# Performance work log

Measured on AMD Instinct MI355X. Metric: run time of the kernel, lower is better.

The kernel has to match this reference:

```python
import jax, jax.numpy as jnp
import numpy as np

TEAM = 5
N_PLAYER = 131072
PD = 256
HD = 256
MLP_H = 512
B = 16384

def _combine(t=TEAM):
    i1, i2 = [], []
    for i in range(t):
        for j in range(t):
            if i != j:
                i1.append(i); i2.append(j)
    return np.array(i1), np.array(i2)

IDX1, IDX2 = _combine()

def setup_inputs() -> dict:
    key = jax.random.key(0)
    ks = jax.random.split(key, 12)
    def xavier(k, shape):
        fan_in, fan_out = shape[1], shape[0]
        std = np.sqrt(2.0 / (fan_in + fan_out))
        return (jax.random.normal(k, shape, dtype=jnp.float32) * std)
    return {
        'team_ids': jax.random.randint(ks[0], (B, TEAM), 0, N_PLAYER),
        'emb': xavier(ks[1], (N_PLAYER, PD)),
        'fm_w1': xavier(ks[2], (2 * HD, PD)),
        'fm_b1': jnp.zeros((2 * HD,), jnp.float32),
        'fm_w2': xavier(ks[3], (HD, 2 * HD)),
        'fm_b2': jnp.zeros((HD,), jnp.float32),
        'att_w': xavier(ks[4], (HD, HD)),
        'att_b': jnp.zeros((HD,), jnp.float32),
        'mlp_w1': xavier(ks[5], (MLP_H, HD)),
        'mlp_b1': jnp.zeros((MLP_H,), jnp.float32),
        'mlp_w2': xavier(ks[6], (1, MLP_H)),
        'mlp_b2': jnp.zeros((1,), jnp.float32),
    }

def reference(team_ids, emb, fm_w1, fm_b1, fm_w2, fm_b2, att_w, att_b,
              mlp_w1, mlp_b1, mlp_w2, mlp_b2):
    # embedding lookup: [B, 5, PD]
    x = emb[team_ids]
    # feature mapper: Linear -> SiLU -> Linear  => [B, 5, HD]
    h = jax.nn.silu(jnp.einsum('btp,hp->bth', x, fm_w1) + fm_b1)
    h = jnp.einsum('bth,oh->bto', h, fm_w2) + fm_b2
    # pairwise gather (20 ordered pairs): [B, 20, HD]
    a = h[:, IDX1]
    b = h[:, IDX2]
    prod = a * b
    # small MLP (dropout is inference identity): [B, 20]
    m = jax.nn.silu(jnp.einsum('bph,mh->bpm', prod, mlp_w1) + mlp_b1)
    order2 = (jnp.einsum('bpm,om->bpo', m, mlp_w2) + mlp_b2)[..., 0]
    # attention (reduce=True -> view [B, 5, 4, HD], softmax over axis 2)
    wa = jnp.einsum('bph,oh->bpo', a, att_w) + att_b
    score = (wa * b).sum(-1).reshape(-1, TEAM, TEAM - 1)
    normal = jax.nn.softmax(score, axis=2).reshape(-1, TEAM * (TEAM - 1))
    order2 = order2 * normal
    return order2.sum(axis=1, keepdims=True)  # [B, 1]
```

## Files before the change

### kernel.cpp

```cpp
#include <hip/hip_runtime.h>

#define NB     16384
#define TEAM   5
#define NPAIR  20
#define UPAIR  10
#define PD     256
#define HD     256
#define H1D    512
#define NPLAY  (NB*TEAM)
#define NCHUNK 4

typedef __attribute__((ext_vector_type(4))) float f32x4;
typedef __attribute__((ext_vector_type(8))) short s16x8;

__device__ __forceinline__ float silu_f(float x){ return x / (1.0f + __expf(-x)); }

__device__ __forceinline__ unsigned short bf16_rne(float x){
  unsigned u = __float_as_uint(x);
  unsigned r = u + 0x7fffu + ((u >> 16) & 1u);
  return (unsigned short)(r >> 16);
}
__device__ __forceinline__ float bf16_to_f(unsigned short s){
  return __uint_as_float(((unsigned)s) << 16);
}

__global__ void k_pack(const float* __restrict__ w, short* __restrict__ wf,
                       int KT, int total)
{
  const int tid = blockIdx.x * 256 + threadIdx.x;
  if (tid >= total) return;
  const int slot = tid & 7;
  const int lane = (tid >> 3) & 63;
  const int grp  = tid >> 9;
  const int kt   = grp % KT;
  const int nt   = grp / KT;
  const int K    = KT * 32;
  const int n = nt * 16 + (lane & 15);
  const int k = kt * 32 + ((lane >> 4) << 3) + slot;
  const float v = w[(size_t)n * K + k];
  const unsigned short hi = bf16_rne(v);
  const float lo = v - bf16_to_f(hi);
  wf[tid]         = (short)hi;
  wf[total + tid] = (short)bf16_rne(lo);
}

__global__ __launch_bounds__(256) void k_fm4(
    const int* __restrict__ tids, const float* __restrict__ emb,
    const short* __restrict__ w1f, const float* __restrict__ b1,
    const short* __restrict__ w2f, const float* __restrict__ b2,
    float* __restrict__ Hout)
{
  __shared__ char smem[65536 + 3072];
  short* Af  = reinterpret_cast<short*>(smem);
  short* H1f = reinterpret_cast<short*>(smem);
  float* Bb  = reinterpret_cast<float*>(smem + 65536);

  const int t = threadIdx.x, lane = t & 63, w = t >> 6;
  const int m0 = blockIdx.x * 32;

  Bb[t]       = b1[t];
  Bb[t + 256] = b1[t + 256];
  Bb[t + 512] = b2[t];

  #pragma unroll
  for (int f = 0; f < 8; ++f) {
    const int g     = t + f * 256;
    const int sg    = (g & 1) * 4;
    const int lane_ = (g >> 1) & 63;
    const int kt_   = (g >> 7) & 7;
    const int mt_   = g >> 10;
    const int p     = mt_ * 16 + (lane_ & 15);
    const int k     = kt_ * 32 + ((lane_ >> 4) << 3) + sg;
    const int row   = tids[m0 + p];
    const float4 a4 = *reinterpret_cast<const float4*>(emb + (size_t)row * PD + k);
    float pv[4] = {a4.x, a4.y, a4.z, a4.w};
    short hi[4], lo[4];
    #pragma unroll
    for (int e = 0; e < 4; ++e) {
      const unsigned short h = bf16_rne(pv[e]);
      hi[e] = (short)h;
      lo[e] = (short)bf16_rne(pv[e] - bf16_to_f(h));
    }
    const int off = ((mt_*8 + kt_)*64 + lane_)*8 + sg;
    *reinterpret_cast<short4*>(&Af[off])        = make_short4(hi[0],hi[1],hi[2],hi[3]);
    *reinterpret_cast<short4*>(&Af[8192 + off]) = make_short4(lo[0],lo[1],lo[2],lo[3]);
  }
  __syncthreads();

  const s16x8* B1 = reinterpret_cast<const s16x8*>(w1f);
  const s16x8* B2 = reinterpret_cast<const s16x8*>(w2f);

  f32x4 acc1[2][8];
  #pragma unroll
  for (int mt = 0; mt < 2; ++mt)
    #pragma unroll
    for (int j = 0; j < 8; ++j) acc1[mt][j] = (f32x4){0.f,0.f,0.f,0.f};

  #pragma unroll
  for (int kt = 0; kt < 8; ++kt) {
    s16x8 ah[2], al[2];
    #pragma unroll
    for (int mt = 0; mt < 2; ++mt) {
      ah[mt] = *reinterpret_cast<const s16x8*>(&Af[((mt*8 + kt)*64 + lane)*8]);
      al[mt] = *reinterpret_cast<const s16x8*>(&Af[8192 + ((mt*8 + kt)*64 + lane)*8]);
    }
    #pragma unroll
    for (int j = 0; j < 8; ++j) {
      const int nt = w * 8 + j;
      const s16x8 bh = B1[(nt*8 + kt)*64 + lane];
      const s16x8 bl = B1[16384 + (nt*8 + kt)*64 + lane];
      #pragma unroll
      for (int mt = 0; mt < 2; ++mt) {
        acc1[mt][j] = __builtin_amdgcn_mfma_f32_16x16x32_bf16(ah[mt], bh, acc1[mt][j], 0,0,0);
        acc1[mt][j] = __builtin_amdgcn_mfma_f32_16x16x32_bf16(al[mt], bh, acc1[mt][j], 0,0,0);
        acc1[mt][j] = __builtin_amdgcn_mfma_f32_16x16x32_bf16(ah[mt], bl, acc1[mt][j], 0,0,0);
      }
    }
  }
  __syncthreads();

  #pragma unroll
  for (int mt = 0; mt < 2; ++mt)
    #pragma unroll
    for (int j = 0; j < 8; ++j) {
      const int n     = w * 128 + j * 16 + (lane & 15);
      const int kt2   = n >> 5;
      const int lhalf = 16 * ((n >> 3) & 3);
      const int slot2 = n & 7;
      #pragma unroll
      for (int r = 0; r < 4; ++r) {
        const int prow = ((lane >> 4) << 2) + r;
        const float v = silu_f(acc1[mt][j][r] + Bb[n]);
        const unsigned short hi = bf16_rne(v);
        const int off = ((mt*16 + kt2)*64 + lhalf + prow)*8 + slot2;
        H1f[off]         = (short)hi;
        H1f[16384 + off] = (short)bf16_rne(v - bf16_to_f(hi));
      }
    }
  __syncthreads();

  f32x4 acc2[2][4];
  #pragma unroll
  for (int mt = 0; mt < 2; ++mt)
    #pragma unroll
    for (int j = 0; j < 4; ++j) acc2[mt][j] = (f32x4){0.f,0.f,0.f,0.f};

  #pragma unroll
  for (int kt = 0; kt < 16; ++kt) {
    s16x8 ah[2], al[2];
    #pragma unroll
    for (int mt = 0; mt < 2; ++mt) {
      ah[mt] = *reinterpret_cast<const s16x8*>(&H1f[((mt*16 + kt)*64 + lane)*8]);
      al[mt] = *reinterpret_cast<const s16x8*>(&H1f[16384 + ((mt*16 + kt)*64 + lane)*8]);
    }
    #pragma unroll
    for (int j = 0; j < 4; ++j) {
      const int nt = w * 4 + j;
      const s16x8 bh = B2[(nt*16 + kt)*64 + lane];
      const s16x8 bl = B2[16384 + (nt*16 + kt)*64 + lane];
      #pragma unroll
      for (int mt = 0; mt < 2; ++mt) {
        acc2[mt][j] = __builtin_amdgcn_mfma_f32_16x16x32_bf16(ah[mt], bh, acc2[mt][j], 0,0,0);
        acc2[mt][j] = __builtin_amdgcn_mfma_f32_16x16x32_bf16(al[mt], bh, acc2[mt][j], 0,0,0);
        acc2[mt][j] = __builtin_amdgcn_mfma_f32_16x16x32_bf16(ah[mt], bl, acc2[mt][j], 0,0,0);
      }
    }
  }

  #pragma unroll
  for (int mt = 0; mt < 2; ++mt)
    #pragma unroll
    for (int j = 0; j < 4; ++j) {
      const int n = w * 64 + j * 16 + (lane & 15);
      #pragma unroll
      for (int r = 0; r < 4; ++r) {
        const int p = m0 + mt*16 + ((lane >> 4) << 2) + r;
        Hout[(size_t)p * PD + n] = acc2[mt][j][r] + Bb[512 + n];
      }
    }
}

__global__ __launch_bounds__(256) void k_score(
    const float* __restrict__ Hin, const short* __restrict__ attf,
    const float* __restrict__ attb, float* __restrict__ SC)
{
  __shared__ char smem[49152 + 1024];
  short* Hf  = reinterpret_cast<short*>(smem);
  float* WAl = reinterpret_cast<float*>(smem);
  float* Ab  = reinterpret_cast<float*>(smem + 49152);

  const int t = threadIdx.x, lane = t & 63, w = t >> 6;
  const int b0 = blockIdx.x * 8;
  const float* src = Hin + (size_t)b0 * TEAM * PD;

  Ab[t] = attb[t];

  #pragma unroll
  for (int f = 0; f < 12; ++f) {
    const int g     = t + f * 256;
    const int sg    = (g & 1) * 4;
    const int lane_ = (g >> 1) & 63;
    const int kt_   = (g >> 7) & 7;
    const int mt_   = g >> 10;
    const int p     = mt_ * 16 + (lane_ & 15);
    const int k     = kt_ * 32 + ((lane_ >> 4) << 3) + sg;
    float4 a4 = make_float4(0.f, 0.f, 0.f, 0.f);
    if (p < 40) a4 = *reinterpret_cast<const float4*>(src + (size_t)p * PD + k);
    float pv[4] = {a4.x, a4.y, a4.z, a4.w};
    short hi[4], lo[4];
    #pragma unroll
    for (int e = 0; e < 4; ++e) {
      const unsigned short h = bf16_rne(pv[e]);
      hi[e] = (short)h;
      lo[e] = (short)bf16_rne(pv[e] - bf16_to_f(h));
    }
    const int off = ((mt_*8 + kt_)*64 + lane_)*8 + sg;
    *reinterpret_cast<short4*>(&Hf[off])         = make_short4(hi[0],hi[1],hi[2],hi[3]);
    *reinterpret_cast<short4*>(&Hf[12288 + off]) = make_short4(lo[0],lo[1],lo[2],lo[3]);
  }
  __syncthreads();

  f32x4 acc[3][4];
  #pragma unroll
  for (int mt = 0; mt < 3; ++mt)
    #pragma unroll
    for (int j = 0; j < 4; ++j) acc[mt][j] = (f32x4){0.f,0.f,0.f,0.f};

  const s16x8* Bh = reinterpret_cast<const s16x8*>(attf);
  #pragma unroll
  for (int kt = 0; kt < 8; ++kt) {
    s16x8 ah[3], al[3];
    #pragma unroll
    for (int mt = 0; mt < 3; ++mt) {
      ah[mt] = *reinterpret_cast<const s16x8*>(&Hf[((mt*8 + kt)*64 + lane)*8]);
      al[mt] = *reinterpret_cast<const s16x8*>(&Hf[12288 + ((mt*8 + kt)*64 + lane)*8]);
    }
    #pragma unroll
    for (int j = 0; j < 4; ++j) {
      const int nt = w * 4 + j;
      const s16x8 bh = Bh[(nt*8 + kt)*64 + lane];
      const s16x8 bl = Bh[8192 + (nt*8 + kt)*64 + lane];
      #pragma unroll
      for (int mt = 0; mt < 3; ++mt) {
        acc[mt][j] = __builtin_amdgcn_mfma_f32_16x16x32_bf16(ah[mt], bh, acc[mt][j], 0,0,0);
        acc[mt][j] = __builtin_amdgcn_mfma_f32_16x16x32_bf16(al[mt], bh, acc[mt][j], 0,0,0);
        acc[mt][j] = __builtin_amdgcn_mfma_f32_16x16x32_bf16(ah[mt], bl, acc[mt][j], 0,0,0);
      }
    }
  }
  __syncthreads();

  #pragma unroll
  for (int mt = 0; mt < 3; ++mt)
    #pragma unroll
    for (int j = 0; j < 4; ++j) {
      const int n = w * 64 + j * 16 + (lane & 15);
      #pragma unroll
      for (int r = 0; r < 4; ++r) {
        const int row = mt * 16 + ((lane >> 4) << 2) + r;
        if (row < 40) WAl[row * 260 + n] = acc[mt][j][r] + Ab[n];
      }
    }
  __syncthreads();

  #pragma unroll
  for (int qq = 0; qq < 2; ++qq) {
    const int q = w * 2 + qq;
    #pragma unroll
    for (int p = 0; p < NPAIR; ++p) {
      const int i1 = p >> 2, jj = p & 3;
      const int i2 = jj + (jj >= i1 ? 1 : 0);
      const float4 a4 = *reinterpret_cast<const float4*>(WAl + (q*TEAM + i1) * 260 + lane * 4);
      const float4 b4 = *reinterpret_cast<const float4*>(src + (size_t)(q*TEAM + i2) * PD + lane * 4);
      float v = a4.x*b4.x + a4.y*b4.y + a4.z*b4.z + a4.w*b4.w;
      #pragma unroll
      for (int off = 32; off > 0; off >>= 1) v += __shfl_xor(v, off);
      if (lane == 0) SC[(size_t)(b0 + q) * NPAIR + p] = v;
    }
  }
}

__global__ __launch_bounds__(256) void k_mlp(
    const float* __restrict__ Hin, const short* __restrict__ w1f,
    const float* __restrict__ b1, const float* __restrict__ w2,
    float* __restrict__ PART)
{
  __shared__ float Hl[40*260];
  __shared__ short Af[2*5*2*512];
  __shared__ float Wb[128];
  __shared__ float Ww[128];

  const int t    = threadIdx.x;
  const int lane = t & 63;
  const int w    = t >> 6;
  const int blkx = blockIdx.x;
  const int cy   = blockIdx.y;
  const int b0   = blkx * 8;

  {
    const float* src = Hin + (size_t)b0 * TEAM * PD;
    #pragma unroll
    for (int rep = 0; rep < 10; ++rep) {
      const int flat = t + rep * 256;
      const int row = flat >> 6, c4 = (flat & 63) * 4;
      *reinterpret_cast<float4*>(Hl + row * 260 + c4) =
        *reinterpret_cast<const float4*>(src + (size_t)row * PD + c4);
    }
    if (t < 128) { Wb[t] = b1[cy * 128 + t]; Ww[t] = w2[cy * 128 + t]; }
  }

  f32x4 acc[5][2];
  #pragma unroll
  for (int mt = 0; mt < 5; ++mt)
    #pragma unroll
    for (int j = 0; j < 2; ++j) acc[mt][j] = (f32x4){0.f,0.f,0.f,0.f};

  const s16x8* Bh = reinterpret_cast<const s16x8*>(w1f);
  const s16x8* Bl = reinterpret_cast<const s16x8*>(w1f + 131072);
  const int nt0 = cy * 8 + w * 2;

  for (int kt = 0; kt < 8; ++kt) {
    const int kc = kt >> 1, ks = kt & 1;
    if (ks == 0) {
      __syncthreads();
      const int kt0 = kc * 64;
      #pragma unroll
      for (int f = 0; f < 5; ++f) {
        const int idx4  = t + f * 256;
        const int sg    = (idx4 & 1) * 4;
        const int lane_ = (idx4 >> 1) & 63;
        const int ks_   = (idx4 >> 7) & 1;
        const int mt_   = idx4 >> 8;
        const int m  = lane_ & 15;
        const int r  = mt_ * 16 + m;
        const int q  = r / UPAIR;
        const int p  = r - q * UPAIR;
        const int i1 = (p >= 4) + (p >= 7) + (p >= 9);
        const int i2 = p - (i1 * (9 - i1)) / 2 + i1 + 1;
        const int kk = kt0 + ks_ * 32 + ((lane_ >> 4) << 3) + sg;
        const float4 a4 = *reinterpret_cast<const float4*>(Hl + (q*TEAM + i1)*260 + kk);
        const float4 b4 = *reinterpret_cast<const float4*>(Hl + (q*TEAM + i2)*260 + kk);
        float pv[4] = {a4.x*b4.x, a4.y*b4.y, a4.z*b4.z, a4.w*b4.w};
        short hi[4], lo[4];
        #pragma unroll
        for (int e = 0; e < 4; ++e) {
          const unsigned short h = bf16_rne(pv[e]);
          hi[e] = (short)h;
          lo[e] = (short)bf16_rne(pv[e] - bf16_to_f(h));
        }
        const int aoff = (mt_ * 2 + ks_) * 512 + lane_ * 8 + sg;
        *reinterpret_cast<short4*>(&Af[aoff])        = make_short4(hi[0],hi[1],hi[2],hi[3]);
        *reinterpret_cast<short4*>(&Af[5120 + aoff]) = make_short4(lo[0],lo[1],lo[2],lo[3]);
      }
      __syncthreads();
    }

    s16x8 ah[5], al[5];
    #pragma unroll
    for (int mt = 0; mt < 5; ++mt) {
      ah[mt] = *reinterpret_cast<const s16x8*>(&Af[(mt*2 + ks)*512 + lane*8]);
      al[mt] = *reinterpret_cast<const s16x8*>(&Af[5120 + (mt*2 + ks)*512 + lane*8]);
    }
    s16x8 bh[2], bl[2];
    #pragma unroll
    for (int j = 0; j < 2; ++j) {
      bh[j] = Bh[((nt0 + j)*8 + kt)*64 + lane];
      bl[j] = Bl[((nt0 + j)*8 + kt)*64 + lane];
    }
    #pragma unroll
    for (int mt = 0; mt < 5; ++mt)
      #pragma unroll
      for (int j = 0; j < 2; ++j) {
        acc[mt][j] = __builtin_amdgcn_mfma_f32_16x16x32_bf16(ah[mt], bh[j], acc[mt][j], 0,0,0);
        acc[mt][j] = __builtin_amdgcn_mfma_f32_16x16x32_bf16(ah[mt], bl[j], acc[mt][j], 0,0,0);
        acc[mt][j] = __builtin_amdgcn_mfma_f32_16x16x32_bf16(al[mt], bh[j], acc[mt][j], 0,0,0);
      }
  }

  __syncthreads();
  float* red = reinterpret_cast<float*>(Af);

  const int colbase = (w * 2) * 16 + (lane & 15);
  #pragma unroll
  for (int mt = 0; mt < 5; ++mt)
    #pragma unroll
    for (int r = 0; r < 4; ++r) {
      float s = 0.0f;
      #pragma unroll
      for (int j = 0; j < 2; ++j) {
        const int c = colbase + j * 16;
        s += silu_f(acc[mt][j][r] + Wb[c]) * Ww[c];
      }
      s += __shfl_xor(s, 1); s += __shfl_xor(s, 2);
      s += __shfl_xor(s, 4); s += __shfl_xor(s, 8);
      if ((lane & 15) == 0) {
        const int row = mt * 16 + ((lane >> 4) << 2) + r;
        red[row * 4 + w] = s;
      }
    }
  __syncthreads();
  if (t < 80) {
    const float s = red[t*4] + red[t*4+1] + red[t*4+2] + red[t*4+3];
    PART[(size_t)cy * (NB*UPAIR) + (size_t)blkx * 80 + t] = s;
  }
}

__global__ void k_final(const float* __restrict__ SC, const float* __restrict__ PART,
                        const float* __restrict__ mb2, float* __restrict__ out)
{
  const int b = blockIdx.x * 256 + threadIdx.x;
  if (b >= NB) return;
  const float bias2 = mb2[0];
  float ord[UPAIR];
  #pragma unroll
  for (int u = 0; u < UPAIR; ++u) {
    float s = bias2;
    #pragma unroll
    for (int g = 0; g < NCHUNK; ++g) s += PART[(size_t)g * (NB*UPAIR) + (size_t)b * UPAIR + u];
    ord[u] = s;
  }
  float sc[NPAIR];
  #pragma unroll
  for (int p = 0; p < NPAIR; ++p) sc[p] = SC[(size_t)b * NPAIR + p];

  float res = 0.0f;
  #pragma unroll
  for (int i = 0; i < TEAM; ++i) {
    float m = sc[4*i];
    #pragma unroll
    for (int jj = 1; jj < 4; ++jj) m = fmaxf(m, sc[4*i + jj]);
    float e[4], d = 0.0f;
    #pragma unroll
    for (int jj = 0; jj < 4; ++jj) { e[jj] = __expf(sc[4*i + jj] - m); d += e[jj]; }
    const float inv = 1.0f / d;
    #pragma unroll
    for (int jj = 0; jj < 4; ++jj) {
      const int i2 = jj + (jj >= i ? 1 : 0);
      const int a  = i < i2 ? i : i2;
      const int bb = i < i2 ? i2 : i;
      const int u  = (a * (9 - a)) / 2 + (bb - a - 1);
      res += ord[u] * e[jj] * inv;
    }
  }
  out[b] = res;
}

extern "C" void kernel_launch(void* const* d_in, const int* in_sizes, int n_in,
                              void* d_out, int out_size, void* d_ws, size_t ws_size,
                              hipStream_t stream)
{
  (void)in_sizes; (void)n_in; (void)out_size; (void)ws_size;
  const int*   tids = (const int*)  d_in[0];
  const float* emb  = (const float*)d_in[1];
  const float* fw1  = (const float*)d_in[2];
  const float* fb1  = (const float*)d_in[3];
  const float* fw2  = (const float*)d_in[4];
  const float* fb2  = (const float*)d_in[5];
  const float* attw = (const float*)d_in[6];
  const float* attb = (const float*)d_in[7];
  const float* mw1  = (const float*)d_in[8];
  const float* mb1  = (const float*)d_in[9];
  const float* mw2  = (const float*)d_in[10];
  const float* mb2  = (const float*)d_in[11];
  float* out = (float*)d_out;

  float* H     = (float*)d_ws;
  float* SC    = H + (size_t)NPLAY * PD;
  float* PART  = SC + (size_t)NB * NPAIR;
  short* w1f_m = (short*)(PART + (size_t)NCHUNK * NB * UPAIR);
  short* w1f_f = w1f_m + 262144;
  short* w2f_f = w1f_f + 262144;
  short* attf  = w2f_f + 262144;

  k_pack<<<512, 256, 0, stream>>>(mw1, w1f_m, 8, 131072);
  k_pack<<<512, 256, 0, stream>>>(fw1, w1f_f, 8, 131072);
  k_pack<<<512, 256, 0, stream>>>(fw2, w2f_f, 16, 131072);
  k_pack<<<256, 256, 0, stream>>>(attw, attf, 8, 65536);
  k_fm4<<<NPLAY/32, 256, 0, stream>>>(tids, emb, w1f_f, fb1, w2f_f, fb2, H);
  k_score<<<NB/8, 256, 0, stream>>>(H, attf, attb, SC);
  k_mlp<<<dim3(NB/8, NCHUNK), 256, 0, stream>>>(H, w1f_m, mb1, mw2, PART);
  k_final<<<NB/256, 256, 0, stream>>>(SC, PART, mb2, out);
}
```

Before: 739.5 us.

## Split fused feature-mapper into two GEMM kernels with an 80-row tile

Replaces the fused two-layer feature-mapper kernel with two kernels: the first computes Linear+SiLU into a global intermediate buffer and the second computes the second Linear. Each uses 80-row tiles with split-bf16 MFMA, and the first layer's output columns are split across two blocks in the y dimension. This is meant to cut per-block shared memory and register pressure and raise occupancy. In exchange it writes and re-reads a 512-wide fp32 intermediate, about 160 MB of global traffic. The fused kernel remains as a fallback when the workspace is too small.

```diff
diff --git a/kernel.cpp b/kernel.cpp
--- a/kernel.cpp
+++ b/kernel.cpp
@@ -42,6 +42,179 @@
   const float lo = v - bf16_to_f(hi);
   wf[tid]         = (short)hi;
   wf[total + tid] = (short)bf16_rne(lo);
+}
+
+__global__ __launch_bounds__(256) void k_l1(
+    const int* __restrict__ tids, const float* __restrict__ emb,
+    const short* __restrict__ w1f, const float* __restrict__ b1,
+    float* __restrict__ Hh1)
+{
+  __shared__ short Af[2*5*2*512];
+  __shared__ float Bb[256];
+  __shared__ int   Tid[80];
+
+  const int t = threadIdx.x, lane = t & 63, w = t >> 6;
+  const int bx = blockIdx.x, cy = blockIdx.y;
+  const int p0 = bx * 80;
+
+  if (t < 80) Tid[t] = tids[p0 + t];
+  Bb[t] = b1[cy * 256 + t];
+
+  f32x4 acc[5][4];
+  #pragma unroll
+  for (int mt = 0; mt < 5; ++mt)
+    #pragma unroll
+    for (int j = 0; j < 4; ++j) acc[mt][j] = (f32x4){0.f,0.f,0.f,0.f};
+
+  const s16x8* Bh = reinterpret_cast<const s16x8*>(w1f);
+
+  for (int kt = 0; kt < 8; ++kt) {
+    const int kc = kt >> 1, ks = kt & 1;
+    if (ks == 0) {
+      __syncthreads();
+      const int kt0 = kc * 64;
+      #pragma unroll
+      for (int f = 0; f < 5; ++f) {
+        const int idx4  = t + f * 256;
+        const int sg    = (idx4 & 1) * 4;
+        const int lane_ = (idx4 >> 1) & 63;
+        const int ks_   = (idx4 >> 7) & 1;
+        const int mt_   = idx4 >> 8;
+        const int p     = mt_ * 16 + (lane_ & 15);
+        const int k     = kt0 + ks_ * 32 + ((lane_ >> 4) << 3) + sg;
+        const int row   = Tid[p];
+        const float4 a4 = *reinterpret_cast<const float4*>(emb + (size_t)row * PD + k);
+        float pv[4] = {a4.x, a4.y, a4.z, a4.w};
+        short hi[4], lo[4];
+        #pragma unroll
+        for (int e = 0; e < 4; ++e) {
+          const unsigned short h = bf16_rne(pv[e]);
+          hi[e] = (short)h;
+          lo[e] = (short)bf16_rne(pv[e] - bf16_to_f(h));
+        }
+        const int aoff = (mt_ * 2 + ks_) * 512 + lane_ * 8 + sg;
+        *reinterpret_cast<short4*>(&Af[aoff])        = make_short4(hi[0],hi[1],hi[2],hi[3]);
+        *reinterpret_cast<short4*>(&Af[5120 + aoff]) = make_short4(lo[0],lo[1],lo[2],lo[3]);
+      }
+      __syncthreads();
+    }
+
+    s16x8 ah[5], al[5];
+    #pragma unroll
+    for (int mt = 0; mt < 5; ++mt) {
+      ah[mt] = *reinterpret_cast<const s16x8*>(&Af[(mt*2 + ks)*512 + lane*8]);
+      al[mt] = *reinterpret_cast<const s16x8*>(&Af[5120 + (mt*2 + ks)*512 + lane*8]);
+    }
+    #pragma unroll
+    for (int j = 0; j < 4; ++j) {
+      const int nt = cy * 16 + w * 4 + j;
+      const s16x8 bh = Bh[(nt*8 + kt)*64 + lane];
+      const s16x8 bl = Bh[16384 + (nt*8 + kt)*64 + lane];
+      #pragma unroll
+      for (int mt = 0; mt < 5; ++mt) {
+        acc[mt][j] = __builtin_amdgcn_mfma_f32_16x16x32_bf16(ah[mt], bh, acc[mt][j], 0,0,0);
+        acc[mt][j] = __builtin_amdgcn_mfma_f32_16x16x32_bf16(al[mt], bh, acc[mt][j], 0,0,0);
+        acc[mt][j] = __builtin_amdgcn_mfma_f32_16x16x32_bf16(ah[mt], bl, acc[mt][j], 0,0,0);
+      }
+    }
+  }
+
+  #pragma unroll
+  for (int mt = 0; mt < 5; ++mt)
+    #pragma unroll
+    for (int j = 0; j < 4; ++j) {
+      const int nl = w * 64 + j * 16 + (lane & 15);
+      const int n  = cy * 256 + nl;
+      #pragma unroll
+      for (int r = 0; r < 4; ++r) {
+        const int p = p0 + mt*16 + ((lane >> 4) << 2) + r;
+        Hh1[(size_t)p * H1D + n] = silu_f(acc[mt][j][r] + Bb[nl]);
+      }
+    }
+}
+
+__global__ __launch_bounds__(256) void k_l2(
+    const float* __restrict__ Hh1, const short* __restrict__ w2f,
+    const float* __restrict__ b2, float* __restrict__ Hout)
+{
+  __shared__ short Af[2*5*2*512];
+  __shared__ float Bb[256];
+
+  const int t = threadIdx.x, lane = t & 63, w = t >> 6;
+  const int bx = blockIdx.x;
+  const int p0 = bx * 80;
+
+  Bb[t] = b2[t];
+
+  f32x4 acc[5][4];
+  #pragma unroll
+  for (int mt = 0; mt < 5; ++mt)
+    #pragma unroll
+    for (int j = 0; j < 4; ++j) acc[mt][j] = (f32x4){0.f,0.f,0.f,0.f};
+
+  const s16x8* B2 = reinterpret_cast<const s16x8*>(w2f);
+
+  for (int kt = 0; kt < 16; ++kt) {
+    const int kc = kt >> 1, ks = kt & 1;
+    if (ks == 0) {
+      __syncthreads();
+      const int kt0 = kc * 64;
+      #pragma unroll
+      for (int f = 0; f < 5; ++f) {
+        const int idx4  = t + f * 256;
+        const int sg    = (idx4 & 1) * 4;
+        const int lane_ = (idx4 >> 1) & 63;
+        const int ks_   = (idx4 >> 7) & 1;
+        const int mt_   = idx4 >> 8;
+        const int p     = p0 + mt_ * 16 + (lane_ & 15);
+        const int k     = kt0 + ks_ * 32 + ((lane_ >> 4) << 3) + sg;
+        const float4 a4 = *reinterpret_cast<const float4*>(Hh1 + (size_t)p * H1D + k);
+        float pv[4] = {a4.x, a4.y, a4.z, a4.w};
+        short hi[4], lo[4];
+        #pragma unroll
+        for (int e = 0; e < 4; ++e) {
+          const unsigned short h = bf16_rne(pv[e]);
+          hi[e] = (short)h;
+          lo[e] = (short)bf16_rne(pv[e] - bf16_to_f(h));
+        }
+        const int aoff = (mt_ * 2 + ks_) * 512 + lane_ * 8 + sg;
+        *reinterpret_cast<short4*>(&Af[aoff])        = make_short4(hi[0],hi[1],hi[2],hi[3]);
+        *reinterpret_cast<short4*>(&Af[5120 + aoff]) = make_short4(lo[0],lo[1],lo[2],lo[3]);
+      }
+      __syncthreads();
+    }
+
+    s16x8 ah[5], al[5];
+    #pragma unroll
+    for (int mt = 0; mt < 5; ++mt) {
+      ah[mt] = *reinterpret_cast<const s16x8*>(&Af[(mt*2 + ks)*512 + lane*8]);
+      al[mt] = *reinterpret_cast<const s16x8*>(&Af[5120 + (mt*2 + ks)*512 + lane*8]);
+    }
+    #pragma unroll
+    for (int j = 0; j < 4; ++j) {
+      const int nt = w * 4 + j;
+      const s16x8 bh = B2[(nt*16 + kt)*64 + lane];
+      const s16x8 bl = B2[16384 + (nt*16 + kt)*64 + lane];
+      #pragma unroll
+      for (int mt = 0; mt < 5; ++mt) {
+        acc[mt][j] = __builtin_amdgcn_mfma_f32_16x16x32_bf16(ah[mt], bh, acc[mt][j], 0,0,0);
+        acc[mt][j] = __builtin_amdgcn_mfma_f32_16x16x32_bf16(al[mt], bh, acc[mt][j], 0,0,0);
+        acc[mt][j] = __builtin_amdgcn_mfma_f32_16x16x32_bf16(ah[mt], bl, acc[mt][j], 0,0,0);
+      }
+    }
+  }
+
+  #pragma unroll
+  for (int mt = 0; mt < 5; ++mt)
+    #pragma unroll
+    for (int j = 0; j < 4; ++j) {
+      const int n = w * 64 + j * 16 + (lane & 15);
+      #pragma unroll
+      for (int r = 0; r < 4; ++r) {
+        const int p = p0 + mt*16 + ((lane >> 4) << 2) + r;
+        Hout[(size_t)p * PD + n] = acc[mt][j][r] + Bb[n];
+      }
+    }
 }
 
 __global__ __launch_bounds__(256) void k_fm4(
@@ -449,7 +622,7 @@
                               void* d_out, int out_size, void* d_ws, size_t ws_size,
                               hipStream_t stream)
 {
-  (void)in_sizes; (void)n_in; (void)out_size; (void)ws_size;
+  (void)in_sizes; (void)n_in; (void)out_size;
   const int*   tids = (const int*)  d_in[0];
   const float* emb  = (const float*)d_in[1];
   const float* fw1  = (const float*)d_in[2];
@@ -471,12 +644,20 @@
   short* w1f_f = w1f_m + 262144;
   short* w2f_f = w1f_f + 262144;
   short* attf  = w2f_f + 262144;
+  float* Hh1   = (float*)(attf + 131072);
+  const size_t NEED = (size_t)((char*)(Hh1 + (size_t)NPLAY * H1D) - (char*)d_ws);
 
   k_pack<<<512, 256, 0, stream>>>(mw1, w1f_m, 8, 131072);
   k_pack<<<512, 256, 0, stream>>>(fw1, w1f_f, 8, 131072);
   k_pack<<<512, 256, 0, stream>>>(fw2, w2f_f, 16, 131072);
   k_pack<<<256, 256, 0, stream>>>(attw, attf, 8, 65536);
-  k_fm4<<<NPLAY/32, 256, 0, stream>>>(tids, emb, w1f_f, fb1, w2f_f, fb2, H);
+
+  if (ws_size >= NEED) {
+    k_l1<<<dim3(NPLAY/80, 2), 256, 0, stream>>>(tids, emb, w1f_f, fb1, Hh1);
+    k_l2<<<NPLAY/80, 256, 0, stream>>>(Hh1, w2f_f, fb2, H);
+  } else {
+    k_fm4<<<NPLAY/32, 256, 0, stream>>>(tids, emb, w1f_f, fb1, w2f_f, fb2, H);
+  }
   k_score<<<NB/8, 256, 0, stream>>>(H, attf, attb, SC);
   k_mlp<<<dim3(NB/8, NCHUNK), 256, 0, stream>>>(H, w1f_m, mb1, mw2, PART);
   k_final<<<NB/256, 256, 0, stream>>>(SC, PART, mb2, out);
```

Result: faster. 665.2 us (-10.0%).
